# Performance work log

Measured on AMD Instinct MI355X. Metric: run time of the kernel, lower is better.

The kernel has to match this reference:

```python
import jax, jax.numpy as jnp
import numpy as np

N_NODES = 50000
N_EDGES = 800000
H = 128       # num_hidden
NUM_INV = 32  # num_inv


def _glorot(key, shape):
    fan_in, fan_out = shape[0], shape[1]
    lim = np.sqrt(6.0 / (fan_in + fan_out)).astype(np.float32)
    return jax.random.uniform(key, shape, jnp.float32, -lim, lim)


def setup_inputs() -> dict:
    key = jax.random.key(0)
    ks = jax.random.split(key, 12)
    x = jax.random.normal(ks[0], (N_NODES, H), jnp.float32)
    adj = jax.random.randint(ks[1], (2, N_EDGES), 0, N_NODES, dtype=jnp.int64)
    inv = jax.random.normal(ks[2], (N_EDGES, NUM_INV), jnp.float32)
    # MessageLayer: message_mlp = Linear(2H+inv -> H), SiLU, Linear(H -> H), SiLU
    Wm1 = _glorot(ks[3], (2 * H + NUM_INV, H)); bm1 = jnp.zeros((H,), jnp.float32)
    Wm2 = _glorot(ks[4], (H, H));               bm2 = jnp.zeros((H,), jnp.float32)
    # edge_inf_mlp = Linear(H -> 1), Sigmoid
    We = _glorot(ks[5], (H, 1));                be = jnp.zeros((1,), jnp.float32)
    # UpdateLayer (num_mes=1): update_mlp = Linear(2H -> H), SiLU, Linear(H -> H)
    Wu1 = _glorot(ks[6], (2 * H, H));           bu1 = jnp.zeros((H,), jnp.float32)
    Wu2 = _glorot(ks[7], (H, H));               bu2 = jnp.zeros((H,), jnp.float32)
    return {"x": x, "adj": adj, "inv": inv,
            "Wm1": Wm1, "bm1": bm1, "Wm2": Wm2, "bm2": bm2,
            "We": We, "be": be,
            "Wu1": Wu1, "bu1": bu1, "Wu2": Wu2, "bu2": bu2}


def reference(x, adj, inv, Wm1, bm1, Wm2, bm2, We, be, Wu1, bu1, Wu2, bu2):
    send, rec = adj[0], adj[1]
    # MessageLayer: gather endpoints, concat with invariants, 2-layer SiLU MLP
    state = jnp.concatenate([x[send], x[rec], inv], axis=1)      # [E, 2H+inv]
    h = jax.nn.silu(state @ Wm1 + bm1)                           # [E, H]
    msg = jax.nn.silu(h @ Wm2 + bm2)                             # [E, H]
    gate = jax.nn.sigmoid(msg @ We + be)                         # [E, 1]
    aggr = jax.ops.segment_sum(msg * gate, rec, num_segments=x.shape[0])  # [N, H]
    # UpdateLayer: concat [x, aggregated message], Linear-SiLU-Linear
    upd_in = jnp.concatenate([x, aggr], axis=1)                  # [N, 2H]
    x_up = jax.nn.silu(upd_in @ Wu1 + bu1) @ Wu2 + bu2           # [N, H]
    # Residual add
    return x + x_up
```

## Files before the change

### kernel.cpp

```cpp
#include <hip/hip_runtime.h>
#include <math.h>

#define NNODES 50000
#define NEDGES 800000
#define HDIM 128
#define NINV 32
#define K1 288
#define NTILES_E 25000
#define NTILES_N 1563

#define W1STRIDE 296
#define U1STRIDE 264
#define HSTRIDE 132
#define FSTRIDE 66

typedef float floatx4 __attribute__((ext_vector_type(4)));
typedef short short8  __attribute__((ext_vector_type(8)));

union V4S8 { uint4 u; short8 s; int2 d[2]; };

__device__ __forceinline__ float silu_f(float z) { return z / (1.0f + __expf(-z)); }

__device__ __forceinline__ unsigned short f2bf_rne(float f) {
    unsigned u = __float_as_uint(f);
    u += 0x7fffu + ((u >> 16) & 1u);
    return (unsigned short)(u >> 16);
}

__device__ __forceinline__ unsigned pk_bf(float hi, float lo) {
    return __builtin_amdgcn_perm(__float_as_uint(hi), __float_as_uint(lo), 0x07060302);
}

__device__ __forceinline__ short8 cvt8(float4 f0, float4 f1) {
    V4S8 v;
    v.u.x = pk_bf(f0.y, f0.x);
    v.u.y = pk_bf(f0.w, f0.z);
    v.u.z = pk_bf(f1.y, f1.x);
    v.u.w = pk_bf(f1.w, f1.z);
    return v.s;
}

__device__ __forceinline__ int adj_at(const void* adj, int is64, long long pos) {
    if (is64) return (int)((const long long*)adj)[pos];
    return ((const int*)adj)[pos];
}

__global__ __launch_bounds__(256) void detect_idx64(const int* __restrict__ adj32,
                                                    int* __restrict__ flag) {
    __shared__ int any_nz;
    if (threadIdx.x == 0) any_nz = 0;
    __syncthreads();
    int v = adj32[threadIdx.x * 2 + 1];
    if (v != 0) atomicOr(&any_nz, 1);
    __syncthreads();
    if (threadIdx.x == 0) *flag = (any_nz == 0) ? 1 : 0;
}

__global__ __launch_bounds__(256) void prep_weights(
    const float* __restrict__ Wm1, const float* __restrict__ Wm2,
    const float* __restrict__ Wu1, const float* __restrict__ Wu2,
    unsigned short* __restrict__ Wm1t, unsigned short* __restrict__ Wm2t,
    unsigned short* __restrict__ Wu1t, unsigned short* __restrict__ Wu2t)
{
    int i = blockIdx.x * 256 + threadIdx.x;
    if (i < 128 * K1) {
        int n = i / K1, k = i % K1;
        Wm1t[i] = f2bf_rne(Wm1[k * HDIM + n]);
    } else if ((i -= 128 * K1) < 128 * HDIM) {
        int n = i / HDIM, k = i % HDIM;
        Wm2t[i] = f2bf_rne(Wm2[k * HDIM + n]);
    } else if ((i -= 128 * HDIM) < 128 * 256) {
        int n = i / 256, k = i % 256;
        Wu1t[i] = f2bf_rne(Wu1[k * HDIM + n]);
    } else if ((i -= 128 * 256) < 128 * HDIM) {
        int n = i / HDIM, k = i % HDIM;
        Wu2t[i] = f2bf_rne(Wu2[k * HDIM + n]);
    }
}

__global__ __launch_bounds__(256) void hist_kernel(const void* __restrict__ adj,
                                                   const int* __restrict__ flagp,
                                                   int* __restrict__ hist)
{
    int e = blockIdx.x * 256 + threadIdx.x;
    if (e < NEDGES) {
        int r = adj_at(adj, *flagp, (long long)NEDGES + e);
        atomicAdd(&hist[r], 1);
    }
}

__global__ __launch_bounds__(1024) void scan_kernel(const int* __restrict__ hist,
                                                    int* __restrict__ cursor)
{
    __shared__ int sums[1024];
    const int t = threadIdx.x;
    const int CH = 49;
    int lo = t * CH; if (lo > NNODES) lo = NNODES;
    int hi = lo + CH; if (hi > NNODES) hi = NNODES;
    int s = 0;
    for (int i = lo; i < hi; ++i) s += hist[i];
    sums[t] = s;
    __syncthreads();
    for (int d = 1; d < 1024; d <<= 1) {
        int v = (t >= d) ? sums[t - d] : 0;
        __syncthreads();
        sums[t] += v;
        __syncthreads();
    }
    int base = (t == 0) ? 0 : sums[t - 1];
    for (int i = lo; i < hi; ++i) { cursor[i] = base; base += hist[i]; }
}

__global__ __launch_bounds__(256) void scatter_kernel(const void* __restrict__ adj,
                                                      const int* __restrict__ flagp,
                                                      int* __restrict__ cursor,
                                                      int* __restrict__ sSend,
                                                      int* __restrict__ sRec,
                                                      int* __restrict__ perm)
{
    int e = blockIdx.x * 256 + threadIdx.x;
    if (e < NEDGES) {
        int is64 = *flagp;
        int s = adj_at(adj, is64, e);
        int r = adj_at(adj, is64, (long long)NEDGES + e);
        int pos = atomicAdd(&cursor[r], 1);
        sSend[pos] = s;
        sRec[pos]  = r;
        perm[pos]  = e;
    }
}

__global__ __launch_bounds__(512, 2) void edge_kernel(
    const float* __restrict__ x, const float* __restrict__ inv,
    const int* __restrict__ sSend, const int* __restrict__ sRec,
    const int* __restrict__ perm,
    const unsigned short* __restrict__ Wm1t, const float* __restrict__ bm1,
    const unsigned short* __restrict__ Wm2t, const float* __restrict__ bm2,
    const float* __restrict__ We, const float* __restrict__ be,
    float* __restrict__ aggr)
{
    __shared__ unsigned short s_w1[128 * W1STRIDE];
    __shared__ unsigned short s_h[8 * 32 * HSTRIDE];
    __shared__ int s_recb[8 * 32];

    const int t    = threadIdx.x;
    const int l    = t & 63;
    const int wid  = t >> 6;
    const int l15  = l & 15;
    const int quad = l >> 4;

    for (int idx = t; idx < 128 * 36; idx += 512) {
        int n = idx / 36, c = idx % 36;
        *(uint4*)&s_w1[n * W1STRIDE + c * 8] = *(const uint4*)(Wm1t + n * K1 + c * 8);
    }

    short8 w2f[4][8];
    #pragma unroll
    for (int ks = 0; ks < 4; ++ks)
        #pragma unroll
        for (int nt = 0; nt < 8; ++nt)
            w2f[ks][nt] = *(const short8*)(Wm2t + (nt * 16 + l15) * HDIM + ks * 32 + quad * 8);

    float wev[8];
    #pragma unroll
    for (int nt = 0; nt < 8; ++nt) wev[nt] = We[nt * 16 + l15];
    const float be0 = be[0];

    __syncthreads();

    unsigned short* hbuf = s_h + wid * (32 * HSTRIDE);
    int* srec = s_recb + wid * 32;
    const int gwave  = blockIdx.x * 8 + wid;
    const int nwaves = gridDim.x * 8;

    for (int tile = gwave; tile < NTILES_E; tile += nwaves) {
        const int e0 = tile * 32;
        int re[2];
        unsigned offS[2], offR[2], offI[2];
        #pragma unroll
        for (int m = 0; m < 2; ++m) {
            int idx = e0 + m * 16 + l15;
            int se  = sSend[idx];
            re[m]   = sRec[idx];
            offS[m] = (unsigned)se * HDIM;
            offR[m] = (unsigned)re[m] * HDIM;
            offI[m] = (unsigned)perm[idx] * NINV;
        }

        auto aptr = [&](int s, int m) -> const float* {
            if (s < 4)  return x   + offS[m] + s * 32 + quad * 8;
            if (s < 8)  return x   + offR[m] + (s - 4) * 32 + quad * 8;
            return             inv + offI[m] + quad * 8;
        };

        float4 F0[2][2], F1[2][2];
        #pragma unroll
        for (int m = 0; m < 2; ++m) {
            const float* p = aptr(0, m); F0[m][0] = ((const float4*)p)[0]; F0[m][1] = ((const float4*)p)[1];
            const float* q = aptr(1, m); F1[m][0] = ((const float4*)q)[0]; F1[m][1] = ((const float4*)q)[1];
        }

        floatx4 acc[2][8];
        #pragma unroll
        for (int nt = 0; nt < 8; ++nt) {
            float bv = bm1[nt * 16 + l15];
            acc[0][nt] = (floatx4){bv, bv, bv, bv};
            acc[1][nt] = acc[0][nt];
        }

        #pragma unroll
        for (int s = 0; s < 9; ++s) {
            short8 a[2];
            #pragma unroll
            for (int m = 0; m < 2; ++m) {
                float4 f0 = (s & 1) ? F1[m][0] : F0[m][0];
                float4 f1 = (s & 1) ? F1[m][1] : F0[m][1];
                a[m] = cvt8(f0, f1);
                if (s + 2 <= 8) {
                    const float* p = aptr(s + 2, m);
                    if (s & 1) { F1[m][0] = ((const float4*)p)[0]; F1[m][1] = ((const float4*)p)[1]; }
                    else       { F0[m][0] = ((const float4*)p)[0]; F0[m][1] = ((const float4*)p)[1]; }
                }
            }
            const unsigned short* wbase = s_w1 + l15 * W1STRIDE + s * 32 + quad * 8;
            #pragma unroll
            for (int nt = 0; nt < 8; ++nt) {
                short8 b = *(const short8*)(wbase + nt * 16 * W1STRIDE);
                acc[0][nt] = __builtin_amdgcn_mfma_f32_16x16x32_bf16(a[0], b, acc[0][nt], 0, 0, 0);
                acc[1][nt] = __builtin_amdgcn_mfma_f32_16x16x32_bf16(a[1], b, acc[1][nt], 0, 0, 0);
            }
        }

        #pragma unroll
        for (int m = 0; m < 2; ++m)
            #pragma unroll
            for (int nt = 0; nt < 8; ++nt)
                #pragma unroll
                for (int r = 0; r < 4; ++r) {
                    float hv = silu_f(acc[m][nt][r]);
                    hbuf[(m * 16 + quad * 4 + r) * HSTRIDE + nt * 16 + l15] =
                        (unsigned short)(__float_as_uint(hv) >> 16);
                }

        #pragma unroll
        for (int nt = 0; nt < 8; ++nt) {
            float bv = bm2[nt * 16 + l15];
            acc[0][nt] = (floatx4){bv, bv, bv, bv};
            acc[1][nt] = acc[0][nt];
        }

        #pragma unroll
        for (int ks = 0; ks < 4; ++ks) {
            short8 a2[2];
            #pragma unroll
            for (int m = 0; m < 2; ++m) {
                int base = (m * 16 + l15) * HSTRIDE + ks * 32 + quad * 8;
                V4S8 v;
                v.d[0] = *(const int2*)(hbuf + base);
                v.d[1] = *(const int2*)(hbuf + base + 4);
                a2[m] = v.s;
            }
            #pragma unroll
            for (int nt = 0; nt < 8; ++nt) {
                acc[0][nt] = __builtin_amdgcn_mfma_f32_16x16x32_bf16(a2[0], w2f[ks][nt], acc[0][nt], 0, 0, 0);
                acc[1][nt] = __builtin_amdgcn_mfma_f32_16x16x32_bf16(a2[1], w2f[ks][nt], acc[1][nt], 0, 0, 0);
            }
        }

        #pragma unroll
        for (int m = 0; m < 2; ++m)
            #pragma unroll
            for (int nt = 0; nt < 8; ++nt)
                #pragma unroll
                for (int r = 0; r < 4; ++r)
                    acc[m][nt][r] = silu_f(acc[m][nt][r]);

        float g[2][4];
        #pragma unroll
        for (int m = 0; m < 2; ++m)
            #pragma unroll
            for (int r = 0; r < 4; ++r) {
                float part = 0.f;
                #pragma unroll
                for (int nt = 0; nt < 8; ++nt)
                    part = fmaf(acc[m][nt][r], wev[nt], part);
                part += __shfl_xor(part, 1);
                part += __shfl_xor(part, 2);
                part += __shfl_xor(part, 4);
                part += __shfl_xor(part, 8);
                g[m][r] = 1.0f / (1.0f + __expf(-(part + be0)));
            }

        if (quad == 0) { srec[l15] = re[0]; srec[16 + l15] = re[1]; }

        float* fred = (float*)hbuf;
        #pragma unroll
        for (int half = 0; half < 2; ++half) {
            #pragma unroll
            for (int m = 0; m < 2; ++m)
                #pragma unroll
                for (int nt2 = 0; nt2 < 4; ++nt2)
                    #pragma unroll
                    for (int r = 0; r < 4; ++r)
                        fred[(m * 16 + quad * 4 + r) * FSTRIDE + nt2 * 16 + l15] =
                            acc[m][half * 4 + nt2][r] * g[m][r];

            float* dstbase = aggr + half * 64 + l;
            float sum = 0.f;
            int prev = srec[0];
            #pragma unroll
            for (int row = 0; row < 32; ++row) {
                float v = fred[row * FSTRIDE + l];
                int rc = srec[row];
                if (rc != prev) {
                    atomicAdd(dstbase + (unsigned)prev * HDIM, sum);
                    sum = 0.f;
                    prev = rc;
                }
                sum += v;
            }
            atomicAdd(dstbase + (unsigned)prev * HDIM, sum);
        }
    }
}

__global__ __launch_bounds__(256) void node_kernel(
    const float* __restrict__ x, const float* __restrict__ aggr,
    const unsigned short* __restrict__ Wu1t, const float* __restrict__ bu1,
    const unsigned short* __restrict__ Wu2t, const float* __restrict__ bu2,
    float* __restrict__ out)
{
    __shared__ unsigned short s_u1[128 * U1STRIDE];
    __shared__ unsigned short s_h[4 * 32 * HSTRIDE];

    const int t    = threadIdx.x;
    const int l    = t & 63;
    const int wid  = t >> 6;
    const int l15  = l & 15;
    const int quad = l >> 4;

    for (int idx = t; idx < 128 * 32; idx += 256) {
        int n = idx / 32, c = idx % 32;
        *(uint4*)&s_u1[n * U1STRIDE + c * 8] = *(const uint4*)(Wu1t + n * 256 + c * 8);
    }

    short8 w2f[4][8];
    #pragma unroll
    for (int ks = 0; ks < 4; ++ks)
        #pragma unroll
        for (int nt = 0; nt < 8; ++nt)
            w2f[ks][nt] = *(const short8*)(Wu2t + (nt * 16 + l15) * HDIM + ks * 32 + quad * 8);

    __syncthreads();

    unsigned short* hbuf = s_h + wid * (32 * HSTRIDE);
    const int tile = blockIdx.x * 4 + wid;
    if (tile >= NTILES_N) return;
    const int n0 = tile * 32;

    unsigned offX[2];
    #pragma unroll
    for (int m = 0; m < 2; ++m) {
        int row = n0 + m * 16 + l15;
        if (row >= NNODES) row = NNODES - 1;
        offX[m] = (unsigned)row * HDIM;
    }

    floatx4 acc[2][8];
    #pragma unroll
    for (int nt = 0; nt < 8; ++nt) {
        float bv = bu1[nt * 16 + l15];
        acc[0][nt] = (floatx4){bv, bv, bv, bv};
        acc[1][nt] = acc[0][nt];
    }

    #pragma unroll
    for (int s = 0; s < 8; ++s) {
        short8 a[2];
        #pragma unroll
        for (int m = 0; m < 2; ++m) {
            const float* p = (s < 4) ? (x + offX[m] + s * 32 + quad * 8)
                                     : (aggr + offX[m] + (s - 4) * 32 + quad * 8);
            float4 f0 = ((const float4*)p)[0];
            float4 f1 = ((const float4*)p)[1];
            a[m] = cvt8(f0, f1);
        }
        const unsigned short* wbase = s_u1 + l15 * U1STRIDE + s * 32 + quad * 8;
        #pragma unroll
        for (int nt = 0; nt < 8; ++nt) {
            short8 b = *(const short8*)(wbase + nt * 16 * U1STRIDE);
            acc[0][nt] = __builtin_amdgcn_mfma_f32_16x16x32_bf16(a[0], b, acc[0][nt], 0, 0, 0);
            acc[1][nt] = __builtin_amdgcn_mfma_f32_16x16x32_bf16(a[1], b, acc[1][nt], 0, 0, 0);
        }
    }

    #pragma unroll
    for (int m = 0; m < 2; ++m)
        #pragma unroll
        for (int nt = 0; nt < 8; ++nt)
            #pragma unroll
            for (int r = 0; r < 4; ++r) {
                float hv = silu_f(acc[m][nt][r]);
                hbuf[(m * 16 + quad * 4 + r) * HSTRIDE + nt * 16 + l15] =
                    (unsigned short)(__float_as_uint(hv) >> 16);
            }

    #pragma unroll
    for (int nt = 0; nt < 8; ++nt) {
        float bv = bu2[nt * 16 + l15];
        acc[0][nt] = (floatx4){bv, bv, bv, bv};
        acc[1][nt] = acc[0][nt];
    }

    #pragma unroll
    for (int ks = 0; ks < 4; ++ks) {
        short8 a2[2];
        #pragma unroll
        for (int m = 0; m < 2; ++m) {
            int base = (m * 16 + l15) * HSTRIDE + ks * 32 + quad * 8;
            V4S8 v;
            v.d[0] = *(const int2*)(hbuf + base);
            v.d[1] = *(const int2*)(hbuf + base + 4);
            a2[m] = v.s;
        }
        #pragma unroll
        for (int nt = 0; nt < 8; ++nt) {
            acc[0][nt] = __builtin_amdgcn_mfma_f32_16x16x32_bf16(a2[0], w2f[ks][nt], acc[0][nt], 0, 0, 0);
            acc[1][nt] = __builtin_amdgcn_mfma_f32_16x16x32_bf16(a2[1], w2f[ks][nt], acc[1][nt], 0, 0, 0);
        }
    }

    #pragma unroll
    for (int m = 0; m < 2; ++m)
        #pragma unroll
        for (int r = 0; r < 4; ++r) {
            int row = n0 + m * 16 + quad * 4 + r;
            if (row < NNODES) {
                #pragma unroll
                for (int nt = 0; nt < 8; ++nt) {
                    int col = nt * 16 + l15;
                    out[(long long)row * HDIM + col] = x[(long long)row * HDIM + col] + acc[m][nt][r];
                }
            }
        }
}

extern "C" void kernel_launch(void* const* d_in, const int* in_sizes, int n_in,
                              void* d_out, int out_size, void* d_ws, size_t ws_size,
                              hipStream_t stream)
{
    const float* x   = (const float*)d_in[0];
    const void*  adj = d_in[1];
    const float* inv = (const float*)d_in[2];
    const float* Wm1 = (const float*)d_in[3];
    const float* bm1 = (const float*)d_in[4];
    const float* Wm2 = (const float*)d_in[5];
    const float* bm2 = (const float*)d_in[6];
    const float* We  = (const float*)d_in[7];
    const float* be  = (const float*)d_in[8];
    const float* Wu1 = (const float*)d_in[9];
    const float* bu1 = (const float*)d_in[10];
    const float* Wu2 = (const float*)d_in[11];
    const float* bu2 = (const float*)d_in[12];
    float* out = (float*)d_out;

    char* ws = (char*)d_ws;
    float* aggr = (float*)ws;
    size_t off = (size_t)NNODES * HDIM * 4;
    int* flag = (int*)(ws + off);            off += 16;
    unsigned short* Wm1t = (unsigned short*)(ws + off);  off += 128 * K1 * 2;
    unsigned short* Wm2t = (unsigned short*)(ws + off);  off += 128 * HDIM * 2;
    unsigned short* Wu1t = (unsigned short*)(ws + off);  off += 128 * 256 * 2;
    unsigned short* Wu2t = (unsigned short*)(ws + off);  off += 128 * HDIM * 2;
    int* hist   = (int*)(ws + off);          off += (size_t)NNODES * 4;
    int* cursor = (int*)(ws + off);          off += (size_t)NNODES * 4;
    int* sSend  = (int*)(ws + off);          off += (size_t)NEDGES * 4;
    int* sRec   = (int*)(ws + off);          off += (size_t)NEDGES * 4;
    int* perm   = (int*)(ws + off);          off += (size_t)NEDGES * 4;

    hipMemsetAsync(aggr, 0, (size_t)NNODES * HDIM * sizeof(float), stream);
    hipMemsetAsync(hist, 0, (size_t)NNODES * sizeof(int), stream);
    detect_idx64<<<1, 256, 0, stream>>>((const int*)adj, flag);
    prep_weights<<<400, 256, 0, stream>>>(Wm1, Wm2, Wu1, Wu2, Wm1t, Wm2t, Wu1t, Wu2t);
    hist_kernel<<<(NEDGES + 255) / 256, 256, 0, stream>>>(adj, flag, hist);
    scan_kernel<<<1, 1024, 0, stream>>>(hist, cursor);
    scatter_kernel<<<(NEDGES + 255) / 256, 256, 0, stream>>>(adj, flag, cursor,
                                                             sSend, sRec, perm);
    edge_kernel<<<256, 512, 0, stream>>>(x, inv, sSend, sRec, perm,
                                         Wm1t, bm1, Wm2t, bm2, We, be, aggr);
    node_kernel<<<(NTILES_N + 3) / 4, 256, 0, stream>>>(x, aggr,
                                                        Wu1t, bu1, Wu2t, bu2, out);
}
```

Baseline: 716.3 us.

## Prefetch next tile's edge gathers across iterations and pack edge indices

The edge kernel now issues the gathers of the next tile's sender and receiver rows during the current tile's layer-2 MLP, so gather latency overlaps with MFMA work. Sorted edge metadata is packed into one int4 per edge instead of three separate arrays. Biases are hoisted into registers, and the Wm2 fragments are reloaded per tile rather than kept live across the loop. The node kernel becomes a persistent grid-stride loop over 256 blocks, and the two memsets are merged by placing hist next to aggr. The cost is higher register pressure from holding 6 prefetched row buffers, which may spill or lower occupancy, plus repeated Wm2 loads from global/L2.

```diff
diff --git a/kernel.cpp b/kernel.cpp
--- a/kernel.cpp
+++ b/kernel.cpp
@@ -114,9 +114,7 @@
 __global__ __launch_bounds__(256) void scatter_kernel(const void* __restrict__ adj,
                                                       const int* __restrict__ flagp,
                                                       int* __restrict__ cursor,
-                                                      int* __restrict__ sSend,
-                                                      int* __restrict__ sRec,
-                                                      int* __restrict__ perm)
+                                                      int4* __restrict__ sEdge)
 {
     int e = blockIdx.x * 256 + threadIdx.x;
     if (e < NEDGES) {
@@ -124,16 +122,13 @@
         int s = adj_at(adj, is64, e);
         int r = adj_at(adj, is64, (long long)NEDGES + e);
         int pos = atomicAdd(&cursor[r], 1);
-        sSend[pos] = s;
-        sRec[pos]  = r;
-        perm[pos]  = e;
+        sEdge[pos] = make_int4(s, r, e, 0);
     }
 }
 
 __global__ __launch_bounds__(512, 2) void edge_kernel(
     const float* __restrict__ x, const float* __restrict__ inv,
-    const int* __restrict__ sSend, const int* __restrict__ sRec,
-    const int* __restrict__ perm,
+    const int4* __restrict__ sEdge,
     const unsigned short* __restrict__ Wm1t, const float* __restrict__ bm1,
     const unsigned short* __restrict__ Wm2t, const float* __restrict__ bm2,
     const float* __restrict__ We, const float* __restrict__ be,
@@ -154,16 +149,13 @@
         *(uint4*)&s_w1[n * W1STRIDE + c * 8] = *(const uint4*)(Wm1t + n * K1 + c * 8);
     }
 
-    short8 w2f[4][8];
+    float bm1v[8], bm2v[8], wev[8];
     #pragma unroll
-    for (int ks = 0; ks < 4; ++ks)
-        #pragma unroll
-        for (int nt = 0; nt < 8; ++nt)
-            w2f[ks][nt] = *(const short8*)(Wm2t + (nt * 16 + l15) * HDIM + ks * 32 + quad * 8);
-
-    float wev[8];
-    #pragma unroll
-    for (int nt = 0; nt < 8; ++nt) wev[nt] = We[nt * 16 + l15];
+    for (int nt = 0; nt < 8; ++nt) {
+        bm1v[nt] = bm1[nt * 16 + l15];
+        bm2v[nt] = bm2[nt * 16 + l15];
+        wev[nt]  = We[nt * 16 + l15];
+    }
     const float be0 = be[0];
 
     __syncthreads();
@@ -172,64 +164,68 @@
     int* srec = s_recb + wid * 32;
     const int gwave  = blockIdx.x * 8 + wid;
     const int nwaves = gridDim.x * 8;
+    if (gwave >= NTILES_E) return;
+
+    int4 eA = sEdge[gwave * 32 + l15];
+    int4 eB = sEdge[gwave * 32 + 16 + l15];
+    unsigned oS0 = (unsigned)eA.x * HDIM, oR0 = (unsigned)eA.y * HDIM, oI0 = (unsigned)eA.z * NINV;
+    unsigned oS1 = (unsigned)eB.x * HDIM, oR1 = (unsigned)eB.y * HDIM, oI1 = (unsigned)eB.z * NINV;
+
+    float4 F[9][2][2];
+    #pragma unroll
+    for (int s = 0; s < 6; ++s) {
+        const float* p0 = (s < 4) ? (x + oS0 + s * 32 + quad * 8) : (x + oR0 + (s - 4) * 32 + quad * 8);
+        const float* p1 = (s < 4) ? (x + oS1 + s * 32 + quad * 8) : (x + oR1 + (s - 4) * 32 + quad * 8);
+        F[s][0][0] = ((const float4*)p0)[0]; F[s][0][1] = ((const float4*)p0)[1];
+        F[s][1][0] = ((const float4*)p1)[0]; F[s][1][1] = ((const float4*)p1)[1];
+    }
 
     for (int tile = gwave; tile < NTILES_E; tile += nwaves) {
-        const int e0 = tile * 32;
-        int re[2];
-        unsigned offS[2], offR[2], offI[2];
-        #pragma unroll
-        for (int m = 0; m < 2; ++m) {
-            int idx = e0 + m * 16 + l15;
-            int se  = sSend[idx];
-            re[m]   = sRec[idx];
-            offS[m] = (unsigned)se * HDIM;
-            offR[m] = (unsigned)re[m] * HDIM;
-            offI[m] = (unsigned)perm[idx] * NINV;
-        }
-
-        auto aptr = [&](int s, int m) -> const float* {
-            if (s < 4)  return x   + offS[m] + s * 32 + quad * 8;
-            if (s < 8)  return x   + offR[m] + (s - 4) * 32 + quad * 8;
-            return             inv + offI[m] + quad * 8;
-        };
-
-        float4 F0[2][2], F1[2][2];
-        #pragma unroll
-        for (int m = 0; m < 2; ++m) {
-            const float* p = aptr(0, m); F0[m][0] = ((const float4*)p)[0]; F0[m][1] = ((const float4*)p)[1];
-            const float* q = aptr(1, m); F1[m][0] = ((const float4*)q)[0]; F1[m][1] = ((const float4*)q)[1];
-        }
+        const int ntile = tile + nwaves;
+        const bool nv = ntile < NTILES_E;
+        int4 nA, nB;
+        if (nv) {
+            nA = sEdge[ntile * 32 + l15];
+            nB = sEdge[ntile * 32 + 16 + l15];
+        }
+        const int re0 = eA.y, re1 = eB.y;
 
         floatx4 acc[2][8];
         #pragma unroll
         for (int nt = 0; nt < 8; ++nt) {
-            float bv = bm1[nt * 16 + l15];
-            acc[0][nt] = (floatx4){bv, bv, bv, bv};
+            acc[0][nt] = (floatx4){bm1v[nt], bm1v[nt], bm1v[nt], bm1v[nt]};
             acc[1][nt] = acc[0][nt];
         }
 
         #pragma unroll
         for (int s = 0; s < 9; ++s) {
-            short8 a[2];
-            #pragma unroll
-            for (int m = 0; m < 2; ++m) {
-                float4 f0 = (s & 1) ? F1[m][0] : F0[m][0];
-                float4 f1 = (s & 1) ? F1[m][1] : F0[m][1];
-                a[m] = cvt8(f0, f1);
-                if (s + 2 <= 8) {
-                    const float* p = aptr(s + 2, m);
-                    if (s & 1) { F1[m][0] = ((const float4*)p)[0]; F1[m][1] = ((const float4*)p)[1]; }
-                    else       { F0[m][0] = ((const float4*)p)[0]; F0[m][1] = ((const float4*)p)[1]; }
-                }
-            }
+            if (s >= 1 && s <= 3) {
+                const int ls = s + 5;
+                const float *p0, *p1;
+                if (ls < 8) { p0 = x + oR0 + (ls - 4) * 32 + quad * 8;
+                              p1 = x + oR1 + (ls - 4) * 32 + quad * 8; }
+                else        { p0 = inv + oI0 + quad * 8;
+                              p1 = inv + oI1 + quad * 8; }
+                F[ls][0][0] = ((const float4*)p0)[0]; F[ls][0][1] = ((const float4*)p0)[1];
+                F[ls][1][0] = ((const float4*)p1)[0]; F[ls][1][1] = ((const float4*)p1)[1];
+            }
+            short8 a0 = cvt8(F[s][0][0], F[s][0][1]);
+            short8 a1 = cvt8(F[s][1][0], F[s][1][1]);
             const unsigned short* wbase = s_w1 + l15 * W1STRIDE + s * 32 + quad * 8;
             #pragma unroll
             for (int nt = 0; nt < 8; ++nt) {
                 short8 b = *(const short8*)(wbase + nt * 16 * W1STRIDE);
-                acc[0][nt] = __builtin_amdgcn_mfma_f32_16x16x32_bf16(a[0], b, acc[0][nt], 0, 0, 0);
-                acc[1][nt] = __builtin_amdgcn_mfma_f32_16x16x32_bf16(a[1], b, acc[1][nt], 0, 0, 0);
-            }
-        }
+                acc[0][nt] = __builtin_amdgcn_mfma_f32_16x16x32_bf16(a0, b, acc[0][nt], 0, 0, 0);
+                acc[1][nt] = __builtin_amdgcn_mfma_f32_16x16x32_bf16(a1, b, acc[1][nt], 0, 0, 0);
+            }
+        }
+
+        short8 w2f[4][8];
+        #pragma unroll
+        for (int ks = 0; ks < 4; ++ks)
+            #pragma unroll
+            for (int nt = 0; nt < 8; ++nt)
+                w2f[ks][nt] = *(const short8*)(Wm2t + (nt * 16 + l15) * HDIM + ks * 32 + quad * 8);
 
         #pragma unroll
         for (int m = 0; m < 2; ++m)
@@ -244,8 +240,7 @@
 
         #pragma unroll
         for (int nt = 0; nt < 8; ++nt) {
-            float bv = bm2[nt * 16 + l15];
-            acc[0][nt] = (floatx4){bv, bv, bv, bv};
+            acc[0][nt] = (floatx4){bm2v[nt], bm2v[nt], bm2v[nt], bm2v[nt]};
             acc[1][nt] = acc[0][nt];
         }
 
@@ -264,6 +259,19 @@
             for (int nt = 0; nt < 8; ++nt) {
                 acc[0][nt] = __builtin_amdgcn_mfma_f32_16x16x32_bf16(a2[0], w2f[ks][nt], acc[0][nt], 0, 0, 0);
                 acc[1][nt] = __builtin_amdgcn_mfma_f32_16x16x32_bf16(a2[1], w2f[ks][nt], acc[1][nt], 0, 0, 0);
+            }
+        }
+
+        if (nv) {
+            eA = nA; eB = nB;
+            oS0 = (unsigned)eA.x * HDIM; oR0 = (unsigned)eA.y * HDIM; oI0 = (unsigned)eA.z * NINV;
+            oS1 = (unsigned)eB.x * HDIM; oR1 = (unsigned)eB.y * HDIM; oI1 = (unsigned)eB.z * NINV;
+            #pragma unroll
+            for (int s = 0; s < 6; ++s) {
+                const float* p0 = (s < 4) ? (x + oS0 + s * 32 + quad * 8) : (x + oR0 + (s - 4) * 32 + quad * 8);
+                const float* p1 = (s < 4) ? (x + oS1 + s * 32 + quad * 8) : (x + oR1 + (s - 4) * 32 + quad * 8);
+                F[s][0][0] = ((const float4*)p0)[0]; F[s][0][1] = ((const float4*)p0)[1];
+                F[s][1][0] = ((const float4*)p1)[0]; F[s][1][1] = ((const float4*)p1)[1];
             }
         }
 
@@ -291,7 +299,7 @@
                 g[m][r] = 1.0f / (1.0f + __expf(-(part + be0)));
             }
 
-        if (quad == 0) { srec[l15] = re[0]; srec[16 + l15] = re[1]; }
+        if (quad == 0) { srec[l15] = re0; srec[16 + l15] = re1; }
 
         float* fred = (float*)hbuf;
         #pragma unroll
@@ -351,98 +359,105 @@
         for (int nt = 0; nt < 8; ++nt)
             w2f[ks][nt] = *(const short8*)(Wu2t + (nt * 16 + l15) * HDIM + ks * 32 + quad * 8);
 
-    __syncthreads();
-
-    unsigned short* hbuf = s_h + wid * (32 * HSTRIDE);
-    const int tile = blockIdx.x * 4 + wid;
-    if (tile >= NTILES_N) return;
-    const int n0 = tile * 32;
-
-    unsigned offX[2];
-    #pragma unroll
-    for (int m = 0; m < 2; ++m) {
-        int row = n0 + m * 16 + l15;
-        if (row >= NNODES) row = NNODES - 1;
-        offX[m] = (unsigned)row * HDIM;
-    }
-
-    floatx4 acc[2][8];
+    float bu1v[8], bu2v[8];
     #pragma unroll
     for (int nt = 0; nt < 8; ++nt) {
-        float bv = bu1[nt * 16 + l15];
-        acc[0][nt] = (floatx4){bv, bv, bv, bv};
-        acc[1][nt] = acc[0][nt];
-    }
-
-    #pragma unroll
-    for (int s = 0; s < 8; ++s) {
-        short8 a[2];
+        bu1v[nt] = bu1[nt * 16 + l15];
+        bu2v[nt] = bu2[nt * 16 + l15];
+    }
+
+    __syncthreads();
+
+    unsigned short* hbuf = s_h + wid * (32 * HSTRIDE);
+    const int nwaves = gridDim.x * 4;
+
+    for (int tile = blockIdx.x * 4 + wid; tile < NTILES_N; tile += nwaves) {
+        const int n0 = tile * 32;
+
+        unsigned offX[2];
         #pragma unroll
         for (int m = 0; m < 2; ++m) {
-            const float* p = (s < 4) ? (x + offX[m] + s * 32 + quad * 8)
-                                     : (aggr + offX[m] + (s - 4) * 32 + quad * 8);
-            float4 f0 = ((const float4*)p)[0];
-            float4 f1 = ((const float4*)p)[1];
-            a[m] = cvt8(f0, f1);
-        }
-        const unsigned short* wbase = s_u1 + l15 * U1STRIDE + s * 32 + quad * 8;
+            int row = n0 + m * 16 + l15;
+            if (row >= NNODES) row = NNODES - 1;
+            offX[m] = (unsigned)row * HDIM;
+        }
+
+        floatx4 acc[2][8];
         #pragma unroll
         for (int nt = 0; nt < 8; ++nt) {
-            short8 b = *(const short8*)(wbase + nt * 16 * U1STRIDE);
-            acc[0][nt] = __builtin_amdgcn_mfma_f32_16x16x32_bf16(a[0], b, acc[0][nt], 0, 0, 0);
-            acc[1][nt] = __builtin_amdgcn_mfma_f32_16x16x32_bf16(a[1], b, acc[1][nt], 0, 0, 0);
-        }
-    }
-
-    #pragma unroll
-    for (int m = 0; m < 2; ++m)
-        #pragma unroll
-        for (int nt = 0; nt < 8; ++nt)
+            acc[0][nt] = (floatx4){bu1v[nt], bu1v[nt], bu1v[nt], bu1v[nt]};
+            acc[1][nt] = acc[0][nt];
+        }
+
+        #pragma unroll
+        for (int s = 0; s < 8; ++s) {
+            short8 a[2];
+            #pragma unroll
+            for (int m = 0; m < 2; ++m) {
+                const float* p = (s < 4) ? (x + offX[m] + s * 32 + quad * 8)
+                                         : (aggr + offX[m] + (s - 4) * 32 + quad * 8);
+                float4 f0 = ((const float4*)p)[0];
+                float4 f1 = ((const float4*)p)[1];
+                a[m] = cvt8(f0, f1);
+            }
+            const unsigned short* wbase = s_u1 + l15 * U1STRIDE + s * 32 + quad * 8;
+            #pragma unroll
+            for (int nt = 0; nt < 8; ++nt) {
+                short8 b = *(const short8*)(wbase + nt * 16 * U1STRIDE);
+                acc[0][nt] = __builtin_amdgcn_mfma_f32_16x16x32_bf16(a[0], b, acc[0][nt], 0, 0, 0);
+                acc[1][nt] = __builtin_amdgcn_mfma_f32_16x16x32_bf16(a[1], b, acc[1][nt], 0, 0, 0);
+            }
+        }
+
+        #pragma unroll
+        for (int m = 0; m < 2; ++m)
+            #pragma unroll
+            for (int nt = 0; nt < 8; ++nt)
+                #pragma unroll
+                for (int r = 0; r < 4; ++r) {
+                    float hv = silu_f(acc[m][nt][r]);
+                    hbuf[(m * 16 + quad * 4 + r) * HSTRIDE + nt * 16 + l15] =
+                        (unsigned short)(__float_as_uint(hv) >> 16);
+                }
+
+        #pragma unroll
+        for (int nt = 0; nt < 8; ++nt) {
+            acc[0][nt] = (floatx4){bu2v[nt], bu2v[nt], bu2v[nt], bu2v[nt]};
+            acc[1][nt] = acc[0][nt];
+        }
+
+        #pragma unroll
+        for (int ks = 0; ks < 4; ++ks) {
+            short8 a2[2];
+            #pragma unroll
+            for (int m = 0; m < 2; ++m) {
+                int base = (m * 16 + l15) * HSTRIDE + ks * 32 + quad * 8;
+                V4S8 v;
+                v.d[0] = *(const int2*)(hbuf + base);
+                v.d[1] = *(const int2*)(hbuf + base + 4);
+                a2[m] = v.s;
+            }
+            #pragma unroll
+            for (int nt = 0; nt < 8; ++nt) {
+                acc[0][nt] = __builtin_amdgcn_mfma_f32_16x16x32_bf16(a2[0], w2f[ks][nt], acc[0][nt], 0, 0, 0);
+                acc[1][nt] = __builtin_amdgcn_mfma_f32_16x16x32_bf16(a2[1], w2f[ks][nt], acc[1][nt], 0, 0, 0);
+            }
+        }
+
+        #pragma unroll
+        for (int m = 0; m < 2; ++m)
             #pragma unroll
             for (int r = 0; r < 4; ++r) {
-                float hv = silu_f(acc[m][nt][r]);
-                hbuf[(m * 16 + quad * 4 + r) * HSTRIDE + nt * 16 + l15] =
-                    (unsigned short)(__float_as_uint(hv) >> 16);
-            }
-
-    #pragma unroll
-    for (int nt = 0; nt < 8; ++nt) {
-        float bv = bu2[nt * 16 + l15];
-        acc[0][nt] = (floatx4){bv, bv, bv, bv};
-        acc[1][nt] = acc[0][nt];
-    }
-
-    #pragma unroll
-    for (int ks = 0; ks < 4; ++ks) {
-        short8 a2[2];
-        #pragma unroll
-        for (int m = 0; m < 2; ++m) {
-            int base = (m * 16 + l15) * HSTRIDE + ks * 32 + quad * 8;
-            V4S8 v;
-            v.d[0] = *(const int2*)(hbuf + base);
-            v.d[1] = *(const int2*)(hbuf + base + 4);
-            a2[m] = v.s;
-        }
-        #pragma unroll
-        for (int nt = 0; nt < 8; ++nt) {
-            acc[0][nt] = __builtin_amdgcn_mfma_f32_16x16x32_bf16(a2[0], w2f[ks][nt], acc[0][nt], 0, 0, 0);
-            acc[1][nt] = __builtin_amdgcn_mfma_f32_16x16x32_bf16(a2[1], w2f[ks][nt], acc[1][nt], 0, 0, 0);
-        }
-    }
-
-    #pragma unroll
-    for (int m = 0; m < 2; ++m)
-        #pragma unroll
-        for (int r = 0; r < 4; ++r) {
-            int row = n0 + m * 16 + quad * 4 + r;
-            if (row < NNODES) {
-                #pragma unroll
-                for (int nt = 0; nt < 8; ++nt) {
-                    int col = nt * 16 + l15;
-                    out[(long long)row * HDIM + col] = x[(long long)row * HDIM + col] + acc[m][nt][r];
+                int row = n0 + m * 16 + quad * 4 + r;
+                if (row < NNODES) {
+                    #pragma unroll
+                    for (int nt = 0; nt < 8; ++nt) {
+                        int col = nt * 16 + l15;
+                        out[(long long)row * HDIM + col] = x[(long long)row * HDIM + col] + acc[m][nt][r];
+                    }
                 }
             }
-        }
+    }
 }
 
 extern "C" void kernel_launch(void* const* d_in, const int* in_sizes, int n_in,
@@ -467,27 +482,22 @@
     char* ws = (char*)d_ws;
     float* aggr = (float*)ws;
     size_t off = (size_t)NNODES * HDIM * 4;
+    int* hist   = (int*)(ws + off);          off += (size_t)NNODES * 4;
     int* flag = (int*)(ws + off);            off += 16;
     unsigned short* Wm1t = (unsigned short*)(ws + off);  off += 128 * K1 * 2;
     unsigned short* Wm2t = (unsigned short*)(ws + off);  off += 128 * HDIM * 2;
     unsigned short* Wu1t = (unsigned short*)(ws + off);  off += 128 * 256 * 2;
     unsigned short* Wu2t = (unsigned short*)(ws + off);  off += 128 * HDIM * 2;
-    int* hist   = (int*)(ws + off);          off += (size_t)NNODES * 4;
     int* cursor = (int*)(ws + off);          off += (size_t)NNODES * 4;
-    int* sSend  = (int*)(ws + off);          off += (size_t)NEDGES * 4;
-    int* sRec   = (int*)(ws + off);          off += (size_t)NEDGES * 4;
-    int* perm   = (int*)(ws + off);          off += (size_t)NEDGES * 4;
-
-    hipMemsetAsync(aggr, 0, (size_t)NNODES * HDIM * sizeof(float), stream);
-    hipMemsetAsync(hist, 0, (size_t)NNODES * sizeof(int), stream);
+    int4* sEdge = (int4*)(ws + off);         off += (size_t)NEDGES * 16;
+
+    hipMemsetAsync(aggr, 0, (size_t)(NNODES * HDIM + NNODES) * sizeof(float), stream);
     detect_idx64<<<1, 256, 0, stream>>>((const int*)adj, flag);
     prep_weights<<<400, 256, 0, stream>>>(Wm1, Wm2, Wu1, Wu2, Wm1t, Wm2t, Wu1t, Wu2t);
     hist_kernel<<<(NEDGES + 255) / 256, 256, 0, stream>>>(adj, flag, hist);
     scan_kernel<<<1, 1024, 0, stream>>>(hist, cursor);
-    scatter_kernel<<<(NEDGES + 255) / 256, 256, 0, stream>>>(adj, flag, cursor,
-                                                             sSend, sRec, perm);
-    edge_kernel<<<256, 512, 0, stream>>>(x, inv, sSend, sRec, perm,
+    scatter_kernel<<<(NEDGES + 255) / 256, 256, 0, stream>>>(adj, flag, cursor, sEdge);
+    edge_kernel<<<256, 512, 0, stream>>>(x, inv, sEdge,
                                          Wm1t, bm1, Wm2t, bm2, We, be, aggr);
-    node_kernel<<<(NTILES_N + 3) / 4, 256, 0, stream>>>(x, aggr,
-                                                        Wu1t, bu1, Wu2t, bu2, out);
-}
+    node_kernel<<<256, 256, 0, stream>>>(x, aggr, Wu1t, bu1, Wu2t, bu2, out);
+}
```

Measured after the change: 832.4 us. +16.2%, slower.
